# Optimization experiments

Hardware: AMD Instinct MI355X
Metric: run time of the kernel (lower is better)

Reference implementation:

```python
import jax, jax.numpy as jnp
import numpy as np
import math

B, L, D = 4, 4096, 1024
H = 16
DH = D // H  # 64
MAX_SEQ = 8192
NF_MAX = MAX_SEQ // 2 + 1  # 4097
EPS = 1e-6
SQRT2_INV = 1.0 / math.sqrt(2.0)


def _ln(x, scale, bias, eps=1e-5):
    m = jnp.mean(x, axis=-1, keepdims=True)
    v = jnp.mean((x - m) ** 2, axis=-1, keepdims=True)
    return (x - m) * jax.lax.rsqrt(v + eps) * scale + bias


def setup_inputs() -> dict:
    key = jax.random.key(0)
    ks = jax.random.split(key, 16)
    s = 0.02
    inp = {
        'x': jax.random.normal(ks[0], (B, L, D), dtype=jnp.float32),
        'Wq': jax.random.normal(ks[1], (D, D), dtype=jnp.float32) * s,
        'Wv': jax.random.normal(ks[2], (D, D), dtype=jnp.float32) * s,
        'Wo': jax.random.normal(ks[3], (D, D), dtype=jnp.float32) * s,
        # gate MLP: LayerNorm(Dh) -> Linear(Dh,4Dh) -> GELU -> Linear(4Dh, 2*NF_MAX)
        'ln_g_s': jnp.ones((DH,), jnp.float32),
        'ln_g_b': jnp.zeros((DH,), jnp.float32),
        'W1': jax.random.normal(ks[4], (4 * DH, DH), dtype=jnp.float32) * s,
        'b1': jnp.zeros((4 * DH,), jnp.float32),
        'W2': jax.random.normal(ks[5], (2 * NF_MAX, 4 * DH), dtype=jnp.float32) * s,
        'b2': jnp.zeros((2 * NF_MAX,), jnp.float32),
        'modrelu_bias': jnp.zeros((H, NF_MAX), jnp.float32),
        # wavelet gating MLP on head_dim
        'ln_w_s': jnp.ones((DH,), jnp.float32),
        'ln_w_b': jnp.zeros((DH,), jnp.float32),
        'Ww1': jax.random.normal(ks[6], (DH, DH), dtype=jnp.float32) * s,
        'bw1': jnp.zeros((DH,), jnp.float32),
        'Ww2': jax.random.normal(ks[7], (DH, DH), dtype=jnp.float32) * s,
        'bw2': jnp.zeros((DH,), jnp.float32),
    }
    return inp


def _spectre_forward(x, Wq, Wv, Wo, ln_g_s, ln_g_b, W1, b1, W2, b2,
                     modrelu_bias, ln_w_s, ln_w_b, Ww1, bw1, Ww2, bw2):
    b, l, d = x.shape
    n_freq = l // 2 + 1
    # projections -> (B,H,L,Dh)
    q = jnp.einsum('bld,ed->ble', x, Wq).reshape(b, l, H, DH).transpose(0, 2, 1, 3)
    v = jnp.einsum('bld,ed->ble', x, Wv).reshape(b, l, H, DH).transpose(0, 2, 1, 3)
    q_bar = jnp.mean(q, axis=2)  # (B,H,Dh) global query
    # frequency gates from global query
    h = _ln(q_bar, ln_g_s, ln_g_b)
    h = jax.nn.gelu(jnp.einsum('bhd,fd->bhf', h, W1) + b1, approximate=False)
    g = jnp.einsum('bhf,gf->bhg', h, W2) + b2  # (B,H,2*NF_MAX)
    gate = g[..., :n_freq] + 1j * g[..., NF_MAX:NF_MAX + n_freq]  # (B,H,n_freq)
    # spectral mixing along sequence axis
    Vf = jnp.fft.rfft(v, axis=2)  # (B,H,n_freq,Dh) complex
    Vf = Vf * gate[..., None]
    # modReLU nonlinearity on complex spectrum
    mag = jnp.abs(Vf)
    bias = modrelu_bias[None, :, :n_freq, None]
    Vf = Vf * (jax.nn.relu(mag + bias) / (mag + EPS))
    y = jnp.fft.irfft(Vf, n=l, axis=2)  # (B,H,L,Dh)
    # wavelet refinement (eval mode -> never skipped)
    gw = _ln(q_bar, ln_w_s, ln_w_b)
    gw = jax.nn.gelu(jnp.einsum('bhd,ed->bhe', gw, Ww1) + bw1, approximate=False)
    gw = jax.nn.sigmoid(jnp.einsum('bhd,ed->bhe', gw, Ww2) + bw2)  # (B,H,Dh)
    yc = y.transpose(0, 1, 3, 2)  # (B,H,Dh,L)
    low = (yc[..., 0::2] + yc[..., 1::2]) * SQRT2_INV   # Haar analysis LP
    high = (yc[..., 1::2] - yc[..., 0::2]) * SQRT2_INV  # Haar analysis HP
    low = low * gw[..., None]
    high = high * gw[..., None]
    even = (low - high) * SQRT2_INV   # Haar synthesis
    odd = (low + high) * SQRT2_INV
    rec = jnp.stack([even, odd], axis=-1).reshape(b, H, DH, l)  # interleave
    y = y + rec.transpose(0, 1, 3, 2)
    out = jnp.einsum('bld,ed->ble', y.transpose(0, 2, 1, 3).reshape(b, l, d), Wo)
    return out


def reference(x, Wq, Wv, Wo, ln_g_s, ln_g_b, W1, b1, W2, b2,
              modrelu_bias, ln_w_s, ln_w_b, Ww1, bw1, Ww2, bw2):
    return _spectre_forward(x, Wq, Wv, Wo, ln_g_s, ln_g_b, W1, b1, W2, b2,
                            modrelu_bias, ln_w_s, ln_w_b, Ww1, bw1, Ww2, bw2)
```

## Files before the change

### kernel.cpp

```cpp
#include <hip/hip_runtime.h>
#include <math.h>

#define LSEQ 4096
#define DDIM 1024
#define NB 4
#define NH 16
#define DHD 64
#define NFREQ 2049
#define NFMAX 4097

typedef __bf16 bf16_8 __attribute__((ext_vector_type(8)));
typedef float f32x4 __attribute__((ext_vector_type(4)));
typedef float f2 __attribute__((ext_vector_type(2)));

__device__ __forceinline__ float gelu_exact(float v) {
    return 0.5f * v * (1.0f + erff(v * 0.70710678118654752440f));
}

__device__ __forceinline__ void gload16(const void* g, void* l) {
    __builtin_amdgcn_global_load_lds((const __attribute__((address_space(1))) char*)g,
                                     (__attribute__((address_space(3))) char*)l, 16, 0, 0);
}

__global__ __launch_bounds__(256) void k_xbar_partial(const float* __restrict__ x, float* __restrict__ xbp,
                                                      __bf16* __restrict__ xbf) {
    int d = blockIdx.x * 256 + threadIdx.x;
    int chunk = blockIdx.y;
    int b = blockIdx.z;
    size_t base = ((size_t)b * LSEQ + (size_t)chunk * 256) * DDIM + d;
    float acc = 0.f;
    for (int l = 0; l < 256; ++l) {
        float v = x[base + (size_t)l * DDIM];
        acc += v;
        xbf[base + (size_t)l * DDIM] = (__bf16)v;
    }
    xbp[(size_t)(b * 16 + chunk) * DDIM + d] = acc;
}

__global__ __launch_bounds__(256) void k_xbar_reduce(const float* __restrict__ xbp, float* __restrict__ xbar) {
    int d = blockIdx.x * 256 + threadIdx.x;
    int b = blockIdx.y;
    float acc = 0.f;
    for (int c = 0; c < 16; ++c) acc += xbp[(size_t)(b * 16 + c) * DDIM + d];
    xbar[b * DDIM + d] = acc * (1.0f / LSEQ);
}

__global__ __launch_bounds__(256) void k_cvt(const float* __restrict__ s, __bf16* __restrict__ d, int n) {
    int i = (blockIdx.x * 256 + threadIdx.x) * 4;
    if (i < n) {
        float4 v = *(const float4*)(s + i);
        d[i] = (__bf16)v.x; d[i + 1] = (__bf16)v.y; d[i + 2] = (__bf16)v.z; d[i + 3] = (__bf16)v.w;
    }
}

__global__ __launch_bounds__(256) void k_qbar(const float* __restrict__ xbar, const float* __restrict__ Wq,
                                              float* __restrict__ qbar) {
    int lane = threadIdx.x & 63;
    int e = blockIdx.x * 4 + (threadIdx.x >> 6);
    const float* wrow = Wq + (size_t)e * DDIM;
    float a0 = 0, a1 = 0, a2 = 0, a3 = 0;
    for (int i = 0; i < 16; ++i) {
        int d = lane + i * 64;
        float w = wrow[d];
        a0 += w * xbar[d];
        a1 += w * xbar[DDIM + d];
        a2 += w * xbar[2 * DDIM + d];
        a3 += w * xbar[3 * DDIM + d];
    }
    for (int off = 32; off > 0; off >>= 1) {
        a0 += __shfl_down(a0, off);
        a1 += __shfl_down(a1, off);
        a2 += __shfl_down(a2, off);
        a3 += __shfl_down(a3, off);
    }
    if (lane == 0) {
        qbar[e] = a0;
        qbar[DDIM + e] = a1;
        qbar[2 * DDIM + e] = a2;
        qbar[3 * DDIM + e] = a3;
    }
}

__global__ __launch_bounds__(256) void k_mlp(const float* __restrict__ qbar,
                                             const float* __restrict__ ln_g_s, const float* __restrict__ ln_g_b,
                                             const float* __restrict__ W1, const float* __restrict__ b1,
                                             const float* __restrict__ ln_w_s, const float* __restrict__ ln_w_b,
                                             const float* __restrict__ Ww1, const float* __restrict__ bw1,
                                             const float* __restrict__ Ww2, const float* __restrict__ bw2,
                                             float* __restrict__ h1g, float* __restrict__ gwp1) {
    int bh = blockIdx.x;
    __shared__ float q[64], hg[64], hw[64], g1[64];
    __shared__ float sm, sv;
    int t = threadIdx.x;
    if (t < 64) q[t] = qbar[bh * 64 + t];
    __syncthreads();
    if (t == 0) {
        float m = 0;
        for (int i = 0; i < 64; ++i) m += q[i];
        m *= (1.0f / 64.0f);
        float v = 0;
        for (int i = 0; i < 64; ++i) { float dd = q[i] - m; v += dd * dd; }
        v *= (1.0f / 64.0f);
        sm = m; sv = v;
    }
    __syncthreads();
    if (t < 64) {
        float n = (q[t] - sm) * rsqrtf(sv + 1e-5f);
        hg[t] = n * ln_g_s[t] + ln_g_b[t];
        hw[t] = n * ln_w_s[t] + ln_w_b[t];
    }
    __syncthreads();
    {
        int f = t;
        const float* w = W1 + (size_t)f * 64;
        float s = b1[f];
        for (int d0 = 0; d0 < 64; ++d0) s += hg[d0] * w[d0];
        h1g[(size_t)bh * 256 + f] = gelu_exact(s);
    }
    if (t < 64) {
        const float* w = Ww1 + (size_t)t * 64;
        float s = bw1[t];
        for (int k = 0; k < 64; ++k) s += hw[k] * w[k];
        g1[t] = gelu_exact(s);
    }
    __syncthreads();
    if (t < 64) {
        const float* w = Ww2 + (size_t)t * 64;
        float s = bw2[t];
        for (int k = 0; k < 64; ++k) s += g1[k] * w[k];
        gwp1[bh * 64 + t] = 1.0f + 1.0f / (1.0f + expf(-s));
    }
}

__global__ __launch_bounds__(256) void k_gate(const float* __restrict__ h1g, const float* __restrict__ W2,
                                              const float* __restrict__ b2,
                                              float* __restrict__ gre, float* __restrict__ gim) {
    int task = blockIdx.x * 4 + (threadIdx.x >> 6);
    if (task >= 2 * NFREQ) return;
    int lane = threadIdx.x & 63;
    int part = task >= NFREQ;
    int f = task - part * NFREQ;
    int row = part ? (NFMAX + f) : f;
    const float* w = W2 + (size_t)row * 256;
    float w0 = w[lane], w1 = w[64 + lane], w2 = w[128 + lane], w3 = w[192 + lane];
    float bias = b2[row];
    float* dst = part ? gim : gre;
    for (int bh = 0; bh < 64; ++bh) {
        const float* hr = h1g + (size_t)bh * 256;
        float p = w0 * hr[lane] + w1 * hr[64 + lane] + w2 * hr[128 + lane] + w3 * hr[192 + lane];
        for (int off = 32; off > 0; off >>= 1) p += __shfl_down(p, off);
        if (lane == 0) dst[(size_t)bh * NFREQ + f] = p + bias;
    }
}

__device__ __forceinline__ void swz256(int bid, int& n0, int& m0, int& b) {
    int w = (bid & 7) * 32 + (bid >> 3);
    b = w >> 6;
    m0 = ((w >> 2) & 15) << 8;
    n0 = (w & 3) << 8;
}

__device__ __forceinline__ void g3_stage_half(const __bf16* __restrict__ src, int row0, int kt,
                                              char* ldshalf, int tid) {
#pragma unroll
    for (int j = 0; j < 2; ++j) {
        int c = j * 512 + tid;
        int r = c >> 3;
        int kc = ((c & 7) ^ (r & 7)) * 8;
        char* dst = ldshalf + (size_t)(j * 512 + (tid & ~63)) * 16;
        gload16(src + ((size_t)(row0 + r) << 10) + kt * 64 + kc, dst);
    }
}

__device__ __forceinline__ void g3_compute(const char* L, int db, int wm, int wn,
                                           int lrow, int lsl, f32x4 (&acc)[8][4]) {
    const char* Ab = L + db * 32768 + wm * 16384;
    const char* Bb = L + 65536 + db * 32768 + (wn >> 1) * 16384;
    int xs = lrow & 7;
    int brb = (wn & 1) * 64;
#pragma unroll
    for (int kk = 0; kk < 2; ++kk) {
        int slot = ((kk * 4 + lsl) ^ xs) << 4;
        bf16_8 af[8], bfr[4];
#pragma unroll
        for (int mi = 0; mi < 8; ++mi)
            af[mi] = *(const bf16_8*)(Ab + (mi * 16 + lrow) * 128 + slot);
#pragma unroll
        for (int ni = 0; ni < 4; ++ni)
            bfr[ni] = *(const bf16_8*)(Bb + (brb + ni * 16 + lrow) * 128 + slot);
        __builtin_amdgcn_s_setprio(1);
#pragma unroll
        for (int mi = 0; mi < 8; ++mi)
#pragma unroll
            for (int ni = 0; ni < 4; ++ni)
                acc[mi][ni] = __builtin_amdgcn_mfma_f32_16x16x32_bf16(af[mi], bfr[ni], acc[mi][ni], 0, 0, 0);
        __builtin_amdgcn_s_setprio(0);
    }
}

__device__ __forceinline__ void g3_core(const __bf16* __restrict__ A, const __bf16* __restrict__ B,
                                        int m0, int n0, char* L, f32x4 (&acc)[8][4]) {
    int tid = threadIdx.x;
    int lane = tid & 63, w = tid >> 6;
    int wm = w >> 2, wn = w & 3;
    int lrow = lane & 15, lsl = lane >> 4;
#pragma unroll
    for (int mi = 0; mi < 8; ++mi)
#pragma unroll
        for (int ni = 0; ni < 4; ++ni) acc[mi][ni] = (f32x4){0.f, 0.f, 0.f, 0.f};

#define G3_STAGE(KT, DB)                                                        \
    do {                                                                        \
        g3_stage_half(A, m0,       (KT), L + (DB) * 32768,               tid);  \
        g3_stage_half(A, m0 + 128, (KT), L + (DB) * 32768 + 16384,       tid);  \
        g3_stage_half(B, n0,       (KT), L + 65536 + (DB) * 32768,       tid);  \
        g3_stage_half(B, n0 + 128, (KT), L + 65536 + (DB) * 32768 + 16384, tid);\
    } while (0)

    G3_STAGE(0, 0);
    G3_STAGE(1, 1);
    asm volatile("s_waitcnt vmcnt(8)" ::: "memory");
    __builtin_amdgcn_s_barrier();
    asm volatile("" ::: "memory");
#pragma unroll 1
    for (int kt = 0; kt < 16; ++kt) {
        int db = kt & 1;
        g3_compute(L, db, wm, wn, lrow, lsl, acc);
        asm volatile("s_waitcnt lgkmcnt(0)" ::: "memory");
        __builtin_amdgcn_s_barrier();
        asm volatile("" ::: "memory");
        if (kt < 14) {
            G3_STAGE(kt + 2, db);
            asm volatile("s_waitcnt vmcnt(8)" ::: "memory");
            __builtin_amdgcn_s_barrier();
            asm volatile("" ::: "memory");
        } else if (kt == 14) {
            asm volatile("s_waitcnt vmcnt(0)" ::: "memory");
            __builtin_amdgcn_s_barrier();
            asm volatile("" ::: "memory");
        }
    }
#undef G3_STAGE
}

__global__ __launch_bounds__(512, 2) void k_vgemm(const __bf16* __restrict__ xbf, const __bf16* __restrict__ Wvb,
                                                  __bf16* __restrict__ vt) {
    __shared__ __align__(16) char L[131072 + 17408];
    __bf16 (*st)[16][68] = (__bf16(*)[16][68])(L + 131072);
    int n0, m0, b;
    swz256(blockIdx.x, n0, m0, b);
    f32x4 acc[8][4];
    g3_core(xbf + ((size_t)b << 22), Wvb, m0, n0, L, acc);
    int tid = threadIdx.x;
    int lane = tid & 63, w = tid >> 6;
    int wm = w >> 2, wn = w & 3;
    size_t vbase = ((size_t)b << 22);
#pragma unroll
    for (int ni = 0; ni < 4; ++ni) {
#pragma unroll
        for (int half = 0; half < 2; ++half) {
#pragma unroll
            for (int ml = 0; ml < 4; ++ml)
#pragma unroll
                for (int r = 0; r < 4; ++r)
                    st[w][lane & 15][ml * 16 + (lane >> 4) * 4 + r] = (__bf16)acc[half * 4 + ml][ni][r];
            asm volatile("" ::: "memory");
#pragma unroll
            for (int er = 0; er < 16; ++er) {
                vt[vbase + (size_t)(n0 + wn * 64 + ni * 16 + er) * LSEQ + m0 + wm * 128 + half * 64 + lane] =
                    st[w][er][lane];
            }
            asm volatile("" ::: "memory");
        }
    }
}

__global__ __launch_bounds__(512, 2) void k_ogemm(const __bf16* __restrict__ ybf, const __bf16* __restrict__ Wob,
                                                  float* __restrict__ out) {
    __shared__ __align__(16) char L[131072];
    int n0, m0, b;
    swz256(blockIdx.x, n0, m0, b);
    f32x4 acc[8][4];
    g3_core(ybf + ((size_t)b << 22), Wob, m0, n0, L, acc);
    int tid = threadIdx.x;
    int lane = tid & 63, w = tid >> 6;
    int wm = w >> 2, wn = w & 3;
    float* ob = out + ((size_t)b << 22);
#pragma unroll
    for (int mi = 0; mi < 8; ++mi)
#pragma unroll
        for (int ni = 0; ni < 4; ++ni)
#pragma unroll
            for (int r = 0; r < 4; ++r)
                ob[(size_t)(m0 + wm * 128 + mi * 16 + (lane >> 4) * 4 + r) * DDIM +
                   n0 + wn * 64 + ni * 16 + (lane & 15)] = acc[mi][ni][r];
}

__device__ __forceinline__ f2 cmul2(f2 a, f2 b) {
    f2 t = a * (f2){b.x, b.x};
    f2 ayx = __builtin_shufflevector(a, a, 1, 0);
    return t + ayx * (f2){-b.y, b.y};
}
__device__ __forceinline__ f2 mulmi(f2 v) {
    f2 s = __builtin_shufflevector(v, v, 1, 0);
    return s * (f2){1.f, -1.f};
}
__device__ __forceinline__ f2 mulpi(f2 v) {
    f2 s = __builtin_shufflevector(v, v, 1, 0);
    return s * (f2){-1.f, 1.f};
}
__device__ __forceinline__ int P8(int i) { return i + (i >> 3) + (i >> 8); }
__device__ __forceinline__ int SR8(int k) {
    return ((k & 7) << 8) | (((k >> 3) & 7) << 5) | (((k >> 6) & 7) << 2) | (k >> 9);
}

template <int S>
__device__ __forceinline__ void dft4v(f2* x) {
    f2 t0 = x[0] + x[2], t1 = x[0] - x[2];
    f2 t2 = x[1] + x[3], t3 = x[1] - x[3];
    f2 j3 = (S == 1) ? mulmi(t3) : mulpi(t3);
    x[0] = t0 + t2;
    x[2] = t0 - t2;
    x[1] = t1 + j3;
    x[3] = t1 - j3;
}

template <int S>
__device__ __forceinline__ void dft8v(f2* x) {
    f2 e[4] = {x[0], x[2], x[4], x[6]};
    f2 o[4] = {x[1], x[3], x[5], x[7]};
    dft4v<S>(e);
    dft4v<S>(o);
    const float c = 0.7071067811865476f;
    const float sg = (S == 1) ? -1.f : 1.f;
    o[1] = cmul2(o[1], (f2){c, sg * c});
    o[2] = (S == 1) ? mulmi(o[2]) : mulpi(o[2]);
    o[3] = cmul2(o[3], (f2){-c, sg * c});
    x[0] = e[0] + o[0];
    x[4] = e[0] - o[0];
    x[1] = e[1] + o[1];
    x[5] = e[1] - o[1];
    x[2] = e[2] + o[2];
    x[6] = e[2] - o[2];
    x[3] = e[3] + o[3];
    x[7] = e[3] - o[3];
}

template <int S>
__device__ __forceinline__ void tw8(f2* x, int j, float invN) {
    float base = ((S == 1) ? -6.283185307179586f : 6.283185307179586f) * invN;
    float sn, cs;
    __sincosf(base * (float)j, &sn, &cs);
    f2 w1 = (f2){cs, sn};
    f2 w2 = cmul2(w1, w1);
    f2 w3 = cmul2(w2, w1);
    f2 w4 = cmul2(w2, w2);
    f2 w5 = cmul2(w4, w1);
    f2 w6 = cmul2(w4, w2);
    f2 w7 = cmul2(w4, w3);
    x[1] = cmul2(x[1], w1);
    x[2] = cmul2(x[2], w2);
    x[3] = cmul2(x[3], w3);
    x[4] = cmul2(x[4], w4);
    x[5] = cmul2(x[5], w5);
    x[6] = cmul2(x[6], w6);
    x[7] = cmul2(x[7], w7);
}

__global__ __launch_bounds__(256, 2) void k_fft(__bf16* __restrict__ vty,
                                                const float* __restrict__ gre, const float* __restrict__ gim,
                                                const float* __restrict__ mrb, const float* __restrict__ gwp1) {
    __shared__ f2 Zp[2312];
    int pid = blockIdx.x;
    int b = pid >> 10, e = pid & 1023;
    int h = e >> 6, dh = e & 63;
    int bh = b * 16 + h;
    size_t gbase = (size_t)bh * NFREQ;
    size_t mbase = (size_t)h * NFMAX;
    __bf16* row = vty + ((size_t)b << 22) + ((size_t)e << 12);
    int t = threadIdx.x;

#pragma unroll
    for (int cc = 0; cc < 2; ++cc) {
        int c = t + cc * 256;
        bf16_8 a = *(const bf16_8*)&row[c * 8];
#pragma unroll
        for (int q = 0; q < 4; ++q)
            Zp[P8(c * 4 + q)] = (f2){(float)a[2 * q], (float)a[2 * q + 1]};
    }
    __syncthreads();

    f2 x[8];
    {
#pragma unroll
        for (int r = 0; r < 8; ++r) x[r] = Zp[P8(r * 256 + t)];
        dft8v<1>(x);
        tw8<1>(x, t, 1.0f / 2048.0f);
#pragma unroll
        for (int r = 0; r < 8; ++r) Zp[P8(r * 256 + t)] = x[r];
    }
    __syncthreads();
    {
        int g = t >> 5, j = t & 31, base = g * 256 + j;
#pragma unroll
        for (int r = 0; r < 8; ++r) x[r] = Zp[P8(base + r * 32)];
        dft8v<1>(x);
        tw8<1>(x, j, 1.0f / 256.0f);
#pragma unroll
        for (int r = 0; r < 8; ++r) Zp[P8(base + r * 32)] = x[r];
    }
    __syncthreads();
    {
        int g = t >> 2, j = t & 3, base = g * 32 + j;
#pragma unroll
        for (int r = 0; r < 8; ++r) x[r] = Zp[P8(base + r * 4)];
        dft8v<1>(x);
        tw8<1>(x, j, 1.0f / 32.0f);
#pragma unroll
        for (int r = 0; r < 8; ++r) Zp[P8(base + r * 4)] = x[r];
    }
    __syncthreads();
    {
        int base = t * 8;
#pragma unroll
        for (int q = 0; q < 4; ++q) { x[q] = Zp[P8(base + q)]; x[4 + q] = Zp[P8(base + 4 + q)]; }
        dft4v<1>(x);
        dft4v<1>(x + 4);
#pragma unroll
        for (int q = 0; q < 4; ++q) { Zp[P8(base + q)] = x[q]; Zp[P8(base + 4 + q)] = x[4 + q]; }
    }
    __syncthreads();

    {
        float sn0, cs0;
        __sincosf(-1.5339807878856412e-3f * (float)(1 + t), &sn0, &cs0);
        f2 wk = (f2){cs0, sn0};
        const f2 W256 = (f2){0.92387953251128675613f, -0.38268343236508977172f};
#pragma unroll
        for (int r = 0; r < 4; ++r) {
            int k = 1 + (r << 8) + t;
            int k2 = 2048 - k;
            int sA = P8(SR8(k)), sB = P8(SR8(k2));
            float cs = wk.x, sn = wk.y;
            f2 Za = Zp[sA], Zb = Zp[sB];
            float Er = 0.5f * (Za.x + Zb.x), Ei = 0.5f * (Za.y - Zb.y);
            float Dr = 0.5f * (Za.x - Zb.x), Di = 0.5f * (Za.y + Zb.y);
            float WDr = cs * Dr - sn * Di, WDi = cs * Di + sn * Dr;
            float Tr = -WDi, Ti = WDr;
            float Vkr = Er - Tr, Vki = Ei - Ti;
            float Vk2r = Er + Tr, Vk2i = -(Ei + Ti);
            float g1r = gre[gbase + k], g1i = gim[gbase + k], b1v = mrb[mbase + k];
            float Ykr = Vkr * g1r - Vki * g1i, Yki = Vkr * g1i + Vki * g1r;
            float m1 = sqrtf(Ykr * Ykr + Yki * Yki);
            float s1 = fmaxf(m1 + b1v, 0.f) / (m1 + 1e-6f);
            Ykr *= s1; Yki *= s1;
            float g2r = gre[gbase + k2], g2i = gim[gbase + k2], b2v = mrb[mbase + k2];
            float Yk2r = Vk2r * g2r - Vk2i * g2i, Yk2i = Vk2r * g2i + Vk2i * g2r;
            float m2 = sqrtf(Yk2r * Yk2r + Yk2i * Yk2i);
            float s2 = fmaxf(m2 + b2v, 0.f) / (m2 + 1e-6f);
            Yk2r *= s2; Yk2i *= s2;
            float Epr = 0.5f * (Ykr + Yk2r), Epi = 0.5f * (Yki - Yk2i);
            float Fr = 0.5f * (Ykr - Yk2r), Fi = 0.5f * (Yki + Yk2i);
            float CWFr = cs * Fr + sn * Fi;
            float CWFi = cs * Fi - sn * Fr;
            Zp[sA] = (f2){Epr - CWFi, Epi + CWFr};
            Zp[sB] = (f2){Epr + CWFi, -Epi + CWFr};
            wk = cmul2(wk, W256);
        }
    }
    if (t == 0) {
        f2 Z0 = Zp[P8(0)];
        float V0 = Z0.x + Z0.y, VN = Z0.x - Z0.y;
        float g0r = gre[gbase], g0i = gim[gbase], b0v = mrb[mbase];
        float y0r = V0 * g0r, y0i = V0 * g0i;
        float m0 = sqrtf(y0r * y0r + y0i * y0i);
        float Y0 = y0r * (fmaxf(m0 + b0v, 0.f) / (m0 + 1e-6f));
        float gNr = gre[gbase + 2048], gNi = gim[gbase + 2048], bNv = mrb[mbase + 2048];
        float yNr = VN * gNr, yNi = VN * gNi;
        float mN = sqrtf(yNr * yNr + yNi * yNi);
        float YN = yNr * (fmaxf(mN + bNv, 0.f) / (mN + 1e-6f));
        Zp[P8(0)] = (f2){0.5f * (Y0 + YN), 0.5f * (Y0 - YN)};
    }
    __syncthreads();

    {
        int base = t * 8;
#pragma unroll
        for (int q = 0; q < 4; ++q) { x[q] = Zp[P8(base + q)]; x[4 + q] = Zp[P8(base + 4 + q)]; }
        dft4v<-1>(x);
        dft4v<-1>(x + 4);
#pragma unroll
        for (int q = 0; q < 4; ++q) { Zp[P8(base + q)] = x[q]; Zp[P8(base + 4 + q)] = x[4 + q]; }
    }
    __syncthreads();
    {
        int g = t >> 2, j = t & 3, base = g * 32 + j;
#pragma unroll
        for (int r = 0; r < 8; ++r) x[r] = Zp[P8(base + r * 4)];
        tw8<-1>(x, j, 1.0f / 32.0f);
        dft8v<-1>(x);
#pragma unroll
        for (int r = 0; r < 8; ++r) Zp[P8(base + r * 4)] = x[r];
    }
    __syncthreads();
    {
        int g = t >> 5, j = t & 31, base = g * 256 + j;
#pragma unroll
        for (int r = 0; r < 8; ++r) x[r] = Zp[P8(base + r * 32)];
        tw8<-1>(x, j, 1.0f / 256.0f);
        dft8v<-1>(x);
#pragma unroll
        for (int r = 0; r < 8; ++r) Zp[P8(base + r * 32)] = x[r];
    }
    __syncthreads();
    {
#pragma unroll
        for (int r = 0; r < 8; ++r) x[r] = Zp[P8(r * 256 + t)];
        tw8<-1>(x, t, 1.0f / 2048.0f);
        dft8v<-1>(x);
        float sc = gwp1[bh * 64 + dh] * (1.0f / 2048.0f);
        unsigned int* row32 = (unsigned int*)row;
#pragma unroll
        for (int r = 0; r < 8; ++r) {
            __bf16 h1 = (__bf16)(x[r].x * sc);
            __bf16 h2 = (__bf16)(x[r].y * sc);
            unsigned int u = (unsigned int)__builtin_bit_cast(unsigned short, h1) |
                             ((unsigned int)__builtin_bit_cast(unsigned short, h2) << 16);
            row32[t + 256 * r] = u;
        }
    }
}

__global__ __launch_bounds__(256) void k_t2(const __bf16* __restrict__ vt, __bf16* __restrict__ ybf) {
    __shared__ __bf16 tl[64][66];
    int e0 = blockIdx.x * 64, l0 = blockIdx.y * 64, b = blockIdx.z;
    int t = threadIdx.x;
    const __bf16* src = vt + ((size_t)b << 22);
    __bf16* dst = ybf + ((size_t)b << 22);
    int er = t >> 3, lc = (t & 7) * 8;
#pragma unroll
    for (int it = 0; it < 2; ++it) {
        int e = er + it * 32;
        bf16_8 v = *(const bf16_8*)&src[(size_t)(e0 + e) * LSEQ + l0 + lc];
#pragma unroll
        for (int j = 0; j < 8; ++j) tl[e][lc + j] = v[j];
    }
    __syncthreads();
    int lr = t >> 3, ec = (t & 7) * 8;
#pragma unroll
    for (int it = 0; it < 2; ++it) {
        int l = lr + it * 32;
        bf16_8 v;
#pragma unroll
        for (int j = 0; j < 8; ++j) v[j] = tl[ec + j][l];
        *(bf16_8*)&dst[(size_t)(l0 + l) * DDIM + e0 + ec] = v;
    }
}

extern "C" void kernel_launch(void* const* d_in, const int* in_sizes, int n_in,
                              void* d_out, int out_size, void* d_ws, size_t ws_size,
                              hipStream_t stream) {
    const float* x      = (const float*)d_in[0];
    const float* Wq     = (const float*)d_in[1];
    const float* Wv     = (const float*)d_in[2];
    const float* Wo     = (const float*)d_in[3];
    const float* ln_g_s = (const float*)d_in[4];
    const float* ln_g_b = (const float*)d_in[5];
    const float* W1     = (const float*)d_in[6];
    const float* b1     = (const float*)d_in[7];
    const float* W2     = (const float*)d_in[8];
    const float* b2     = (const float*)d_in[9];
    const float* mrb    = (const float*)d_in[10];
    const float* ln_w_s = (const float*)d_in[11];
    const float* ln_w_b = (const float*)d_in[12];
    const float* Ww1    = (const float*)d_in[13];
    const float* bw1    = (const float*)d_in[14];
    const float* Ww2    = (const float*)d_in[15];
    const float* bw2    = (const float*)d_in[16];
    float* out = (float*)d_out;

    char* W = (char*)d_ws;
    __bf16* xbf = (__bf16*)W;
    __bf16* ybf = xbf;
    __bf16* Wvb = (__bf16*)(W + 33554432);
    __bf16* Wob = (__bf16*)(W + 35651584);
    float*  xbp = (float*)(W + 37748736);
    float*  xbar= (float*)(W + 38010880);
    float*  qbar= (float*)(W + 38027264);
    float*  h1g = (float*)(W + 38043648);
    float*  gwp1= (float*)(W + 38109184);
    float*  gre = (float*)(W + 38125568);
    float*  gim = (float*)(W + 38650112);

    __bf16* vt = (__bf16*)d_out;

    k_xbar_partial<<<dim3(4, 16, 4), 256, 0, stream>>>(x, xbp, xbf);
    k_cvt<<<1024, 256, 0, stream>>>(Wv, Wvb, DDIM * DDIM);
    k_cvt<<<1024, 256, 0, stream>>>(Wo, Wob, DDIM * DDIM);
    k_xbar_reduce<<<dim3(4, 4), 256, 0, stream>>>(xbp, xbar);
    k_qbar<<<256, 256, 0, stream>>>(xbar, Wq, qbar);
    k_mlp<<<64, 256, 0, stream>>>(qbar, ln_g_s, ln_g_b, W1, b1, ln_w_s, ln_w_b,
                                  Ww1, bw1, Ww2, bw2, h1g, gwp1);
    k_gate<<<1025, 256, 0, stream>>>(h1g, W2, b2, gre, gim);
    k_vgemm<<<256, 512, 0, stream>>>(xbf, Wvb, vt);
    k_fft<<<4096, 256, 0, stream>>>(vt, gre, gim, mrb, gwp1);
    k_t2<<<dim3(16, 64, 4), 256, 0, stream>>>(vt, ybf);
    k_ogemm<<<256, 512, 0, stream>>>(ybf, Wob, out);
}
```

Baseline: 193.9 us.

## Switch GEMM core to 4-stage K=32 pipeline with single barrier per step

```diff
diff --git a/kernel.cpp b/kernel.cpp
--- a/kernel.cpp
+++ b/kernel.cpp
@@ -160,87 +160,87 @@
     n0 = (w & 3) << 8;
 }
 
-__device__ __forceinline__ void g3_stage_half(const __bf16* __restrict__ src, int row0, int kt,
-                                              char* ldshalf, int tid) {
+__device__ __forceinline__ void g4_stage(const __bf16* __restrict__ src, int row0, int kt,
+                                         char* buf, int tid) {
 #pragma unroll
     for (int j = 0; j < 2; ++j) {
         int c = j * 512 + tid;
-        int r = c >> 3;
-        int kc = ((c & 7) ^ (r & 7)) * 8;
-        char* dst = ldshalf + (size_t)(j * 512 + (tid & ~63)) * 16;
-        gload16(src + ((size_t)(row0 + r) << 10) + kt * 64 + kc, dst);
-    }
-}
-
-__device__ __forceinline__ void g3_compute(const char* L, int db, int wm, int wn,
-                                           int lrow, int lsl, f32x4 (&acc)[8][4]) {
-    const char* Ab = L + db * 32768 + wm * 16384;
-    const char* Bb = L + 65536 + db * 32768 + (wn >> 1) * 16384;
-    int xs = lrow & 7;
-    int brb = (wn & 1) * 64;
-#pragma unroll
-    for (int kk = 0; kk < 2; ++kk) {
-        int slot = ((kk * 4 + lsl) ^ xs) << 4;
-        bf16_8 af[8], bfr[4];
-#pragma unroll
-        for (int mi = 0; mi < 8; ++mi)
-            af[mi] = *(const bf16_8*)(Ab + (mi * 16 + lrow) * 128 + slot);
+        int q = c >> 3, p = c & 7;
+        int s3 = p ^ (q & 7);
+        int r = 2 * q + (s3 >> 2);
+        int kc = (s3 & 3) * 8;
+        char* dst = buf + (size_t)(j * 512 + (tid & ~63)) * 16;
+        gload16(src + ((size_t)(row0 + r) << 10) + kt * 32 + kc, dst);
+    }
+}
+
+__device__ __forceinline__ void g4_compute(const char* L, int bi, int wm, int wn,
+                                           int lane, f32x4 (&acc)[8][4]) {
+    int lrow = lane & 15, lsl = lane >> 4;
+    const char* Ab = L + bi * 16384;
+    const char* Bb = L + 65536 + bi * 16384;
+    int s3 = (lrow & 1) * 4 + lsl;
+    bf16_8 af[8], bfr[4];
+#pragma unroll
+    for (int mi = 0; mi < 8; ++mi) {
+        int q = wm * 64 + mi * 8 + (lrow >> 1);
+        af[mi] = *(const bf16_8*)(Ab + q * 128 + ((s3 ^ (q & 7)) << 4));
+    }
+#pragma unroll
+    for (int ni = 0; ni < 4; ++ni) {
+        int q = wn * 32 + ni * 8 + (lrow >> 1);
+        bfr[ni] = *(const bf16_8*)(Bb + q * 128 + ((s3 ^ (q & 7)) << 4));
+    }
+    __builtin_amdgcn_s_setprio(1);
+#pragma unroll
+    for (int mi = 0; mi < 8; ++mi)
 #pragma unroll
         for (int ni = 0; ni < 4; ++ni)
-            bfr[ni] = *(const bf16_8*)(Bb + (brb + ni * 16 + lrow) * 128 + slot);
-        __builtin_amdgcn_s_setprio(1);
-#pragma unroll
-        for (int mi = 0; mi < 8; ++mi)
-#pragma unroll
-            for (int ni = 0; ni < 4; ++ni)
-                acc[mi][ni] = __builtin_amdgcn_mfma_f32_16x16x32_bf16(af[mi], bfr[ni], acc[mi][ni], 0, 0, 0);
-        __builtin_amdgcn_s_setprio(0);
-    }
-}
-
-__device__ __forceinline__ void g3_core(const __bf16* __restrict__ A, const __bf16* __restrict__ B,
+            acc[mi][ni] = __builtin_amdgcn_mfma_f32_16x16x32_bf16(af[mi], bfr[ni], acc[mi][ni], 0, 0, 0);
+    __builtin_amdgcn_s_setprio(0);
+}
+
+__device__ __forceinline__ void g4_core(const __bf16* __restrict__ A, const __bf16* __restrict__ B,
                                         int m0, int n0, char* L, f32x4 (&acc)[8][4]) {
     int tid = threadIdx.x;
     int lane = tid & 63, w = tid >> 6;
     int wm = w >> 2, wn = w & 3;
-    int lrow = lane & 15, lsl = lane >> 4;
 #pragma unroll
     for (int mi = 0; mi < 8; ++mi)
 #pragma unroll
         for (int ni = 0; ni < 4; ++ni) acc[mi][ni] = (f32x4){0.f, 0.f, 0.f, 0.f};
 
-#define G3_STAGE(KT, DB)                                                        \
-    do {                                                                        \
-        g3_stage_half(A, m0,       (KT), L + (DB) * 32768,               tid);  \
-        g3_stage_half(A, m0 + 128, (KT), L + (DB) * 32768 + 16384,       tid);  \
-        g3_stage_half(B, n0,       (KT), L + 65536 + (DB) * 32768,       tid);  \
-        g3_stage_half(B, n0 + 128, (KT), L + 65536 + (DB) * 32768 + 16384, tid);\
+#define G4_STAGE(KT, BI)                                   \
+    do {                                                   \
+        g4_stage(A, m0, (KT), L + (BI) * 16384, tid);      \
+        g4_stage(B, n0, (KT), L + 65536 + (BI) * 16384, tid); \
     } while (0)
 
-    G3_STAGE(0, 0);
-    G3_STAGE(1, 1);
+    G4_STAGE(0, 0);
+    G4_STAGE(1, 1);
+    G4_STAGE(2, 2);
     asm volatile("s_waitcnt vmcnt(8)" ::: "memory");
     __builtin_amdgcn_s_barrier();
     asm volatile("" ::: "memory");
 #pragma unroll 1
-    for (int kt = 0; kt < 16; ++kt) {
-        int db = kt & 1;
-        g3_compute(L, db, wm, wn, lrow, lsl, acc);
+    for (int kt = 0; kt < 32; ++kt) {
+        int bi = kt & 3;
+        if (kt < 29) {
+            G4_STAGE(kt + 3, (kt + 3) & 3);
+        }
+        g4_compute(L, bi, wm, wn, lane, acc);
         asm volatile("s_waitcnt lgkmcnt(0)" ::: "memory");
+        if (kt <= 28) {
+            asm volatile("s_waitcnt vmcnt(8)" ::: "memory");
+        } else if (kt == 29) {
+            asm volatile("s_waitcnt vmcnt(4)" ::: "memory");
+        } else if (kt == 30) {
+            asm volatile("s_waitcnt vmcnt(0)" ::: "memory");
+        }
         __builtin_amdgcn_s_barrier();
         asm volatile("" ::: "memory");
-        if (kt < 14) {
-            G3_STAGE(kt + 2, db);
-            asm volatile("s_waitcnt vmcnt(8)" ::: "memory");
-            __builtin_amdgcn_s_barrier();
-            asm volatile("" ::: "memory");
-        } else if (kt == 14) {
-            asm volatile("s_waitcnt vmcnt(0)" ::: "memory");
-            __builtin_amdgcn_s_barrier();
-            asm volatile("" ::: "memory");
-        }
-    }
-#undef G3_STAGE
+    }
+#undef G4_STAGE
 }
 
 __global__ __launch_bounds__(512, 2) void k_vgemm(const __bf16* __restrict__ xbf, const __bf16* __restrict__ Wvb,
@@ -250,7 +250,7 @@
     int n0, m0, b;
     swz256(blockIdx.x, n0, m0, b);
     f32x4 acc[8][4];
-    g3_core(xbf + ((size_t)b << 22), Wvb, m0, n0, L, acc);
+    g4_core(xbf + ((size_t)b << 22), Wvb, m0, n0, L, acc);
     int tid = threadIdx.x;
     int lane = tid & 63, w = tid >> 6;
     int wm = w >> 2, wn = w & 3;
@@ -281,7 +281,7 @@
     int n0, m0, b;
     swz256(blockIdx.x, n0, m0, b);
     f32x4 acc[8][4];
-    g3_core(ybf + ((size_t)b << 22), Wob, m0, n0, L, acc);
+    g4_core(ybf + ((size_t)b << 22), Wob, m0, n0, L, acc);
     int tid = threadIdx.x;
     int lane = tid & 63, w = tid >> 6;
     int wm = w >> 2, wn = w & 3;
```

New measurement: 194.3 us. No clear change (+0.2%).
